# Kernel tuning notes

Measured on AMD Instinct MI355X. Metric: run time of the kernel, lower is better.

The kernel has to match this reference:

```python
import jax, jax.numpy as jnp
import numpy as np

MAX_THRESHOLD = 0.25  # init kwarg
B, S, D, E = 8, 4096, 512, 8


def setup_inputs() -> dict:
    key = jax.random.key(0)
    ks = jax.random.split(key, 5)
    scale = 1.0 / np.sqrt(D)
    return {
        "inputs": jax.random.normal(ks[0], (B, S, D), dtype=jnp.float32),
        "W_gate": jax.random.normal(ks[1], (D, E), dtype=jnp.float32) * scale,
        "b_gate": jnp.zeros((E,), dtype=jnp.float32),
        "W_thr": jax.random.normal(ks[2], (D, 1), dtype=jnp.float32) * scale,
        "b_thr": jnp.zeros((1,), dtype=jnp.float32),
        "W_exp": jax.random.normal(ks[3], (E, D, D), dtype=jnp.float32) * scale,
        "b_exp": jnp.zeros((E, D), dtype=jnp.float32),
    }


def reference(inputs, W_gate, b_gate, W_thr, b_thr, W_exp, b_exp):
    d = inputs.shape[-1]
    x = inputs.reshape(-1, d)  # [T, D]
    # gating
    gate_logits = jax.nn.softmax(x @ W_gate + b_gate, axis=-1)          # [T, E]
    thresholds = jax.nn.sigmoid(x @ W_thr + b_thr) * MAX_THRESHOLD      # [T, 1]
    adapted = gate_logits - thresholds                                  # [T, E]
    selected = (adapted >= 0).astype(x.dtype)                           # [T, E]
    weights = adapted * selected                                        # [T, E]
    wsum = jnp.sum(weights, axis=-1, keepdims=True)
    wsum = jnp.where(wsum == 0, jnp.ones_like(wsum), wsum)
    weights = weights / wsum
    # dense-equivalent of gather->expert->scatter (weights are 0 where unselected)
    ex_out = jnp.einsum('td,edf->etf', x, W_exp) + b_exp[:, None, :]    # [E, T, D]
    results = jnp.einsum('etf,te->tf', ex_out, weights)                 # [T, D]
    return results.reshape(inputs.shape[:-1] + (results.shape[-1],))
```

## Files before the change

kernel.cpp:

```cpp
#include <hip/hip_runtime.h>


#define T_TOKENS 32768
#define DDIM 512
#define KDIM 4096
#define SLOTB 16384
#define SLOTA 16384

typedef __attribute__((ext_vector_type(8))) short short8;
typedef __attribute__((ext_vector_type(4))) float floatx4;
typedef __bf16 bf16x2 __attribute__((ext_vector_type(2)));

__device__ __forceinline__ unsigned short f2bf(float f) {
    unsigned int u = __float_as_uint(f);
    u += 0x7FFFu + ((u >> 16) & 1u);
    return (unsigned short)(u >> 16);
}

__device__ __forceinline__ unsigned int pk2(float a, float b) {
#if __has_builtin(__builtin_amdgcn_cvt_pk_bf16_f32)
    bf16x2 v = __builtin_amdgcn_cvt_pk_bf16_f32(a, b);
    return __builtin_bit_cast(unsigned int, v);
#else
    return (unsigned int)f2bf(a) | ((unsigned int)f2bf(b) << 16);
#endif
}

__device__ __forceinline__ void async_copy16(const void* g, void* l) {
    __builtin_amdgcn_global_load_lds(
        (const __attribute__((address_space(1))) void*)g,
        (__attribute__((address_space(3))) void*)l, 16, 0, 0);
}

__device__ __forceinline__ unsigned int scale_pair(unsigned int u, float w) {
    float lo = __uint_as_float(u << 16) * w;
    float hi = __uint_as_float(u & 0xFFFF0000u) * w;
    return pk2(lo, hi);
}

__global__ __launch_bounds__(256) void gating_cvt_bt(
    const float* __restrict__ x, const float* __restrict__ Wg,
    const float* __restrict__ bg, const float* __restrict__ Wt,
    const float* __restrict__ bt, float* __restrict__ wbuf,
    unsigned short* __restrict__ Xbf,
    const float* __restrict__ Wexp, unsigned short* __restrict__ Bt)
{
    const int tid = threadIdx.x;

    if (blockIdx.x >= 512) {
        __shared__ float tile[64][65];
        const int bb = blockIdx.x - 512;
        const int k0 = (bb & 63) * 64;
        const int n0 = (bb >> 6) * 64;
        const int r = tid >> 4, cq = tid & 15;
#pragma unroll
        for (int p = 0; p < 4; ++p) {
            const int rr = p * 16 + r;
            const float4 v = *(const float4*)(Wexp + (size_t)(k0 + rr) * 512 + n0 + cq * 4);
            tile[rr][cq * 4 + 0] = v.x;
            tile[rr][cq * 4 + 1] = v.y;
            tile[rr][cq * 4 + 2] = v.z;
            tile[rr][cq * 4 + 3] = v.w;
        }
        __syncthreads();
        const int rn = tid >> 2;
        const int kq = tid & 3;
        alignas(16) unsigned short buf[16];
#pragma unroll
        for (int j = 0; j < 16; ++j) buf[j] = f2bf(tile[kq * 16 + j][rn]);
        unsigned short* dst = Bt + (size_t)(n0 + rn) * KDIM + k0 + kq * 16;
        *(uint4*)(dst) = *(const uint4*)(buf);
        *(uint4*)(dst + 8) = *(const uint4*)(buf + 8);
        return;
    }

    const int wv = tid >> 6;
    const int lane = tid & 63;

    float4 wg[16];
    {
        const float4* wgp = (const float4*)(Wg + lane * 64);
#pragma unroll
        for (int c = 0; c < 16; ++c) wg[c] = wgp[c];
    }
    const float4 wt0 = *(const float4*)(Wt + lane * 8);
    const float4 wt1 = *(const float4*)(Wt + lane * 8 + 4);
    const float bgv[8] = {bg[0], bg[1], bg[2], bg[3], bg[4], bg[5], bg[6], bg[7]};
    const float btv = bt[0];

    for (int it = 0; it < 16; ++it) {
        const int t = blockIdx.x * 64 + wv * 16 + it;
        const float* xp = x + (size_t)t * 512 + lane * 8;
        const float4 a0 = *(const float4*)(xp);
        const float4 a1 = *(const float4*)(xp + 4);

        uint2 pk0, pk1;
        pk0.x = pk2(a0.x, a0.y);
        pk0.y = pk2(a0.z, a0.w);
        pk1.x = pk2(a1.x, a1.y);
        pk1.y = pk2(a1.z, a1.w);
        uint2* xd = (uint2*)(Xbf + (size_t)t * 512 + lane * 8);
        xd[0] = pk0;
        xd[1] = pk1;

        const float xv[8] = {a0.x, a0.y, a0.z, a0.w, a1.x, a1.y, a1.z, a1.w};
        const float wtv[8] = {wt0.x, wt0.y, wt0.z, wt0.w, wt1.x, wt1.y, wt1.z, wt1.w};
        float g[9];
#pragma unroll
        for (int e = 0; e < 9; ++e) g[e] = 0.f;
#pragma unroll
        for (int j = 0; j < 8; ++j) {
            const float4 wlo = wg[j * 2];
            const float4 whi = wg[j * 2 + 1];
            g[0] = fmaf(xv[j], wlo.x, g[0]);
            g[1] = fmaf(xv[j], wlo.y, g[1]);
            g[2] = fmaf(xv[j], wlo.z, g[2]);
            g[3] = fmaf(xv[j], wlo.w, g[3]);
            g[4] = fmaf(xv[j], whi.x, g[4]);
            g[5] = fmaf(xv[j], whi.y, g[5]);
            g[6] = fmaf(xv[j], whi.z, g[6]);
            g[7] = fmaf(xv[j], whi.w, g[7]);
            g[8] = fmaf(xv[j], wtv[j], g[8]);
        }
#pragma unroll
        for (int e = 0; e < 9; ++e) {
            g[e] += __shfl_xor(g[e], 1);
            g[e] += __shfl_xor(g[e], 2);
            g[e] += __shfl_xor(g[e], 4);
            g[e] += __shfl_xor(g[e], 8);
            g[e] += __shfl_xor(g[e], 16);
            g[e] += __shfl_xor(g[e], 32);
        }
        if (lane == 0) {
#pragma unroll
            for (int e = 0; e < 8; ++e) g[e] += bgv[e];
            g[8] += btv;
            float m = g[0];
#pragma unroll
            for (int e = 1; e < 8; ++e) m = fmaxf(m, g[e]);
            float s = 0.f;
            float p[8];
#pragma unroll
            for (int e = 0; e < 8; ++e) { p[e] = __expf(g[e] - m); s += p[e]; }
            const float inv = 1.f / s;
            const float thr = 0.25f / (1.f + __expf(-g[8]));
            float w8[8];
            float ws = 0.f;
#pragma unroll
            for (int e = 0; e < 8; ++e) {
                float a = p[e] * inv - thr;
                w8[e] = a > 0.f ? a : 0.f;
                ws += w8[e];
            }
            if (ws == 0.f) ws = 1.f;
            const float invw = 1.f / ws;
            float4 o0, o1;
            o0.x = w8[0] * invw; o0.y = w8[1] * invw; o0.z = w8[2] * invw; o0.w = w8[3] * invw;
            o1.x = w8[4] * invw; o1.y = w8[5] * invw; o1.z = w8[6] * invw; o1.w = w8[7] * invw;
            float4* op = (float4*)(wbuf + (size_t)t * 8);
            op[0] = o0;
            op[1] = o1;
        }
    }
}

__global__ __launch_bounds__(512, 2) void moe_gemm(
    const unsigned short* __restrict__ Xbf, const float* __restrict__ wbuf,
    const float* __restrict__ bexp, const unsigned short* __restrict__ Bt,
    float* __restrict__ out)
{
    __shared__ alignas(16) unsigned short Bs[3 * SLOTB];
    __shared__ alignas(16) unsigned short As[SLOTA];
    __shared__ float sWbT[8 * 256];

    const int tid = threadIdx.x;
    const int wave = tid >> 6;
    const int lane = tid & 63;
    const int wm = wave >> 2;
    const int wn = wave & 3;
    const int lm = lane & 15;
    const int lq = lane >> 4;
    const int brow = lane >> 3;
    const int cg = (lane & 7) ^ brow;
    const int c8 = tid & 7;
    const int r0 = tid >> 3;
    const int swzA = ((c8 ^ (r0 & 7)) << 3);

    const int lin = blockIdx.x;
    const int g = lin & 7;
    const int j_ = lin >> 3;
    const int t0 = (g * 16 + (j_ >> 1)) * 256;
    const int n0 = (j_ & 1) * 256;

    {
        const int row = tid & 255, pr = tid >> 8;
        const float4 w4 = *(const float4*)(wbuf + (size_t)(t0 + row) * 8 + pr * 4);
        sWbT[(pr * 4 + 0) * 256 + row] = w4.x;
        sWbT[(pr * 4 + 1) * 256 + row] = w4.y;
        sWbT[(pr * 4 + 2) * 256 + row] = w4.z;
        sWbT[(pr * 4 + 3) * 256 + row] = w4.w;
    }

#define STAGE_B(s_, slot_, i0, i1)                                              \
    {                                                                           \
        const int k0_ = (s_) << 6;                                              \
        _Pragma("unroll")                                                       \
        for (int i = (i0); i < (i1); ++i)                                       \
            async_copy16(Bt + (size_t)(n0 + wave * 32 + i * 8 + brow) * KDIM + k0_ + cg * 8, \
                         Bs + (slot_) * SLOTB + (wave * 32 + i * 8) * 64);      \
    }
#define LOADA_ISSUE(s_)                                                         \
    {                                                                           \
        const int d0_ = ((s_) & 7) << 6;                                        \
        _Pragma("unroll")                                                       \
        for (int m = 0; m < 4; ++m)                                             \
            ar[m] = *(const uint4*)(Xbf + (size_t)(t0 + r0 + m * 64) * 512 + d0_ + c8 * 8); \
    }
#define ASCALE_WRITE(s_)                                                        \
    {                                                                           \
        const int e1 = (s_) >> 3;                                               \
        _Pragma("unroll")                                                       \
        for (int m = 0; m < 4; ++m) {                                           \
            const float w = sWbT[e1 * 256 + r0 + m * 64];                       \
            uint4 o;                                                            \
            o.x = scale_pair(ar[m].x, w);                                       \
            o.y = scale_pair(ar[m].y, w);                                       \
            o.z = scale_pair(ar[m].z, w);                                       \
            o.w = scale_pair(ar[m].w, w);                                       \
            *(uint4*)(As + (r0 + m * 64) * 64 + swzA) = o;                      \
        }                                                                       \
    }
#define READ_A(ih)                                                              \
    {                                                                           \
        _Pragma("unroll")                                                       \
        for (int ii = 0; ii < 4; ++ii)                                          \
            _Pragma("unroll")                                                   \
            for (int kk = 0; kk < 2; ++kk) {                                    \
                const int row = wm * 128 + ((ih) * 4 + ii) * 16 + lm;           \
                const int ch = kk * 4 + lq;                                     \
                af[ii][kk] = *(const short8*)(As + row * 64 + ((ch ^ (row & 7)) << 3)); \
            }                                                                   \
    }
#define READ_B(q_, dst)                                                         \
    {                                                                           \
        _Pragma("unroll")                                                       \
        for (int jj = 0; jj < 2; ++jj)                                          \
            _Pragma("unroll")                                                   \
            for (int kk = 0; kk < 2; ++kk) {                                    \
                const int row = wn * 64 + ((q_) * 2 + jj) * 16 + lm;            \
                const int ch = kk * 4 + lq;                                     \
                dst[jj][kk] = *(const short8*)(Bb + row * 64 + ((ch ^ (row & 7)) << 3)); \
            }                                                                   \
    }
#define MFMA_Q(ih, q_, bq)                                                      \
    {                                                                           \
        __builtin_amdgcn_s_setprio(1);                                          \
        _Pragma("unroll")                                                       \
        for (int ii = 0; ii < 4; ++ii)                                          \
            _Pragma("unroll")                                                   \
            for (int jj = 0; jj < 2; ++jj)                                      \
                _Pragma("unroll")                                               \
                for (int kk = 0; kk < 2; ++kk)                                  \
                    acc[(ih) * 4 + ii][(q_) * 2 + jj] =                         \
                        __builtin_amdgcn_mfma_f32_16x16x32_bf16(                \
                            af[ii][kk], bq[jj][kk], acc[(ih) * 4 + ii][(q_) * 2 + jj], 0, 0, 0); \
        __builtin_amdgcn_s_setprio(0);                                          \
    }

    floatx4 acc[8][4];
#pragma unroll
    for (int i = 0; i < 8; ++i)
#pragma unroll
        for (int j = 0; j < 4; ++j) acc[i][j] = (floatx4){0.f, 0.f, 0.f, 0.f};

    uint4 ar[4];

    LOADA_ISSUE(0);
    STAGE_B(0, 0, 0, 4);
    STAGE_B(1, 1, 0, 4);
    asm volatile("s_waitcnt vmcnt(8)" ::: "memory");
    ASCALE_WRITE(0);
    asm volatile("s_waitcnt vmcnt(4) lgkmcnt(0)" ::: "memory");
    __builtin_amdgcn_s_barrier();

    int sB = 0;
    for (int s = 0; s < 64; ++s) {
        const int sB1 = (sB == 2) ? 0 : sB + 1;
        const int sB2 = (sB == 0) ? 2 : sB - 1;
        const unsigned short* Bb = Bs + sB * SLOTB;
        short8 af[4][2], b0[2][2], b1[2][2];

        READ_A(0);
        READ_B(0, b0);
        if (s < 63) LOADA_ISSUE(s + 1);
        __builtin_amdgcn_s_barrier();
        MFMA_Q(0, 0, b0);
        __builtin_amdgcn_s_barrier();

        READ_B(1, b1);
        if (s < 62) STAGE_B(s + 2, sB2, 0, 2);
        __builtin_amdgcn_s_barrier();
        MFMA_Q(0, 1, b1);
        __builtin_amdgcn_s_barrier();

        READ_A(1);
        if (s < 62) STAGE_B(s + 2, sB2, 2, 4);
        __builtin_amdgcn_s_barrier();
        MFMA_Q(1, 1, b1);
        __builtin_amdgcn_s_barrier();

        if (s < 62) {
            asm volatile("s_waitcnt vmcnt(4)" ::: "memory");
        } else if (s == 62) {
            asm volatile("s_waitcnt vmcnt(0)" ::: "memory");
        }
        if (s < 63) ASCALE_WRITE(s + 1);
        READ_B(0, b0);
        __builtin_amdgcn_s_barrier();
        MFMA_Q(1, 0, b0);
        asm volatile("s_waitcnt lgkmcnt(0)" ::: "memory");
        __builtin_amdgcn_s_barrier();

        sB = sB1;
    }

    float bc[4][8];
#pragma unroll
    for (int j = 0; j < 4; ++j) {
        const int col = n0 + wn * 64 + j * 16 + lm;
#pragma unroll
        for (int e = 0; e < 8; ++e) bc[j][e] = bexp[e * 512 + col];
    }
#pragma unroll
    for (int i = 0; i < 8; ++i)
#pragma unroll
        for (int r = 0; r < 4; ++r) {
            const int rowl = wm * 128 + i * 16 + lq * 4 + r;
            const float4 w0 = *(const float4*)(wbuf + (size_t)(t0 + rowl) * 8);
            const float4 w1 = *(const float4*)(wbuf + (size_t)(t0 + rowl) * 8 + 4);
            float* op = out + (size_t)(t0 + rowl) * 512 + n0 + wn * 64 + lm;
#pragma unroll
            for (int j = 0; j < 4; ++j) {
                float bias = w0.x * bc[j][0];
                bias = fmaf(w0.y, bc[j][1], bias);
                bias = fmaf(w0.z, bc[j][2], bias);
                bias = fmaf(w0.w, bc[j][3], bias);
                bias = fmaf(w1.x, bc[j][4], bias);
                bias = fmaf(w1.y, bc[j][5], bias);
                bias = fmaf(w1.z, bc[j][6], bias);
                bias = fmaf(w1.w, bc[j][7], bias);
                op[j * 16] = acc[i][j][r] + bias;
            }
        }
#undef STAGE_B
#undef LOADA_ISSUE
#undef ASCALE_WRITE
#undef READ_A
#undef READ_B
#undef MFMA_Q
}

extern "C" void kernel_launch(void* const* d_in, const int* in_sizes, int n_in,
                              void* d_out, int out_size, void* d_ws, size_t ws_size,
                              hipStream_t stream) {
    const float* x   = (const float*)d_in[0];
    const float* Wg  = (const float*)d_in[1];
    const float* bg  = (const float*)d_in[2];
    const float* Wt  = (const float*)d_in[3];
    const float* bt  = (const float*)d_in[4];
    const float* Wex = (const float*)d_in[5];
    const float* bex = (const float*)d_in[6];
    float* out = (float*)d_out;

    unsigned short* Xbf = (unsigned short*)d_ws;
    unsigned short* Bt  = (unsigned short*)((char*)d_ws + (size_t)T_TOKENS * DDIM * 2);
    float* wbuf = (float*)((char*)d_ws + (size_t)T_TOKENS * DDIM * 2
                                       + (size_t)DDIM * KDIM * 2);

    gating_cvt_bt<<<1024, 256, 0, stream>>>(x, Wg, bg, Wt, bt, wbuf, Xbf, Wex, Bt);
    moe_gemm<<<256, 512, 0, stream>>>(Xbf, wbuf, bex, Bt, out);
}
```

Measured before the change: 282.7 us.

## Halve GEMM K-step to 32 with double-buffered A and smaller LDS slots

Restructures the MoE GEMM main loop from 64 steps of K=64 into 128 steps of K=32. The B tile keeps three slots and the scaled A tile now has two slots, each half the previous size, with a new 4-chunk XOR swizzle. LDS use drops from about 136 KB to about 88 KB, and each step runs two MFMA halves with fewer barriers per step. This cuts shared memory pressure, which may allow two blocks per CU, at the cost of twice as many loop iterations and synchronisation points.

Result: slower. 310.2 us (+9.7%).

```diff
diff --git a/kernel.cpp b/kernel.cpp
--- a/kernel.cpp
+++ b/kernel.cpp
@@ -4,8 +4,7 @@
 #define T_TOKENS 32768
 #define DDIM 512
 #define KDIM 4096
-#define SLOTB 16384
-#define SLOTA 16384
+#define SLOT32 8192
 
 typedef __attribute__((ext_vector_type(8))) short short8;
 typedef __attribute__((ext_vector_type(4))) float floatx4;
@@ -169,8 +168,8 @@
     const float* __restrict__ bexp, const unsigned short* __restrict__ Bt,
     float* __restrict__ out)
 {
-    __shared__ alignas(16) unsigned short Bs[3 * SLOTB];
-    __shared__ alignas(16) unsigned short As[SLOTA];
+    __shared__ alignas(16) unsigned short Bs[3 * SLOT32];
+    __shared__ alignas(16) unsigned short Asl[2 * SLOT32];
     __shared__ float sWbT[8 * 256];
 
     const int tid = threadIdx.x;
@@ -180,11 +179,10 @@
     const int wn = wave & 3;
     const int lm = lane & 15;
     const int lq = lane >> 4;
-    const int brow = lane >> 3;
-    const int cg = (lane & 7) ^ brow;
-    const int c8 = tid & 7;
-    const int r0 = tid >> 3;
-    const int swzA = ((c8 ^ (r0 & 7)) << 3);
+    const int srow = wave * 16 + (lane >> 2);
+    const int pc = lane & 3;
+    const int cgk = pc ^ ((lane >> 3) & 3);
+    const int prd = lq ^ ((lm >> 1) & 3);
 
     const int lin = blockIdx.x;
     const int g = lin & 7;
@@ -201,69 +199,59 @@
         sWbT[(pr * 4 + 3) * 256 + row] = w4.w;
     }
 
-#define STAGE_B(s_, slot_, i0, i1)                                              \
-    {                                                                           \
-        const int k0_ = (s_) << 6;                                              \
-        _Pragma("unroll")                                                       \
-        for (int i = (i0); i < (i1); ++i)                                       \
-            async_copy16(Bt + (size_t)(n0 + wave * 32 + i * 8 + brow) * KDIM + k0_ + cg * 8, \
-                         Bs + (slot_) * SLOTB + (wave * 32 + i * 8) * 64);      \
-    }
-#define LOADA_ISSUE(s_)                                                         \
-    {                                                                           \
-        const int d0_ = ((s_) & 7) << 6;                                        \
-        _Pragma("unroll")                                                       \
-        for (int m = 0; m < 4; ++m)                                             \
-            ar[m] = *(const uint4*)(Xbf + (size_t)(t0 + r0 + m * 64) * 512 + d0_ + c8 * 8); \
-    }
-#define ASCALE_WRITE(s_)                                                        \
-    {                                                                           \
-        const int e1 = (s_) >> 3;                                               \
-        _Pragma("unroll")                                                       \
-        for (int m = 0; m < 4; ++m) {                                           \
-            const float w = sWbT[e1 * 256 + r0 + m * 64];                       \
+#define STAGE_B(s_, slot_)                                                      \
+    {                                                                           \
+        _Pragma("unroll")                                                       \
+        for (int i = 0; i < 2; ++i)                                             \
+            async_copy16(Bt + (size_t)(n0 + i * 128 + srow) * KDIM + (s_) * 32 + cgk * 8, \
+                         Bs + (slot_) * SLOT32 + (i * 128 + wave * 16) * 32);   \
+    }
+#define LOADA(s_)                                                               \
+    {                                                                           \
+        const int d0_ = ((s_) & 15) << 5;                                       \
+        _Pragma("unroll")                                                       \
+        for (int i = 0; i < 2; ++i)                                             \
+            ar[i] = *(const uint4*)(Xbf + (size_t)(t0 + i * 128 + srow) * 512 + d0_ + pc * 8); \
+    }
+#define AWRITE(s_)                                                              \
+    {                                                                           \
+        const int e1 = (s_) >> 4;                                               \
+        _Pragma("unroll")                                                       \
+        for (int i = 0; i < 2; ++i) {                                           \
+            const float w = sWbT[e1 * 256 + i * 128 + srow];                    \
             uint4 o;                                                            \
-            o.x = scale_pair(ar[m].x, w);                                       \
-            o.y = scale_pair(ar[m].y, w);                                       \
-            o.z = scale_pair(ar[m].z, w);                                       \
-            o.w = scale_pair(ar[m].w, w);                                       \
-            *(uint4*)(As + (r0 + m * 64) * 64 + swzA) = o;                      \
+            o.x = scale_pair(ar[i].x, w);                                       \
+            o.y = scale_pair(ar[i].y, w);                                       \
+            o.z = scale_pair(ar[i].z, w);                                       \
+            o.w = scale_pair(ar[i].w, w);                                       \
+            *(uint4*)(Asl + ((s_) & 1) * SLOT32 + (i * 128 + srow) * 32 + cgk * 8) = o; \
         }                                                                       \
     }
-#define READ_A(ih)                                                              \
-    {                                                                           \
+#define READ_AF(ih)                                                             \
+    {                                                                           \
+        _Pragma("unroll")                                                       \
+        for (int ii = 0; ii < 4; ++ii) {                                        \
+            const int row = wm * 128 + ((ih) * 4 + ii) * 16 + lm;               \
+            af[ii] = *(const short8*)(Ab + row * 32 + prd * 8);                 \
+        }                                                                       \
+    }
+#define READ_B()                                                                \
+    {                                                                           \
+        _Pragma("unroll")                                                       \
+        for (int j = 0; j < 4; ++j) {                                           \
+            const int row = wn * 64 + j * 16 + lm;                              \
+            b[j] = *(const short8*)(Bb + row * 32 + prd * 8);                   \
+        }                                                                       \
+    }
+#define MFMA_H(ih)                                                              \
+    {                                                                           \
+        __builtin_amdgcn_s_setprio(1);                                          \
         _Pragma("unroll")                                                       \
         for (int ii = 0; ii < 4; ++ii)                                          \
             _Pragma("unroll")                                                   \
-            for (int kk = 0; kk < 2; ++kk) {                                    \
-                const int row = wm * 128 + ((ih) * 4 + ii) * 16 + lm;           \
-                const int ch = kk * 4 + lq;                                     \
-                af[ii][kk] = *(const short8*)(As + row * 64 + ((ch ^ (row & 7)) << 3)); \
-            }                                                                   \
-    }
-#define READ_B(q_, dst)                                                         \
-    {                                                                           \
-        _Pragma("unroll")                                                       \
-        for (int jj = 0; jj < 2; ++jj)                                          \
-            _Pragma("unroll")                                                   \
-            for (int kk = 0; kk < 2; ++kk) {                                    \
-                const int row = wn * 64 + ((q_) * 2 + jj) * 16 + lm;            \
-                const int ch = kk * 4 + lq;                                     \
-                dst[jj][kk] = *(const short8*)(Bb + row * 64 + ((ch ^ (row & 7)) << 3)); \
-            }                                                                   \
-    }
-#define MFMA_Q(ih, q_, bq)                                                      \
-    {                                                                           \
-        __builtin_amdgcn_s_setprio(1);                                          \
-        _Pragma("unroll")                                                       \
-        for (int ii = 0; ii < 4; ++ii)                                          \
-            _Pragma("unroll")                                                   \
-            for (int jj = 0; jj < 2; ++jj)                                      \
-                _Pragma("unroll")                                               \
-                for (int kk = 0; kk < 2; ++kk)                                  \
-                    acc[(ih) * 4 + ii][(q_) * 2 + jj] =                         \
-                        __builtin_amdgcn_mfma_f32_16x16x32_bf16(                \
-                            af[ii][kk], bq[jj][kk], acc[(ih) * 4 + ii][(q_) * 2 + jj], 0, 0, 0); \
+            for (int j = 0; j < 4; ++j)                                         \
+                acc[(ih) * 4 + ii][j] = __builtin_amdgcn_mfma_f32_16x16x32_bf16( \
+                    af[ii], b[j], acc[(ih) * 4 + ii][j], 0, 0, 0);              \
         __builtin_amdgcn_s_setprio(0);                                          \
     }
 
@@ -273,55 +261,44 @@
 #pragma unroll
         for (int j = 0; j < 4; ++j) acc[i][j] = (floatx4){0.f, 0.f, 0.f, 0.f};
 
-    uint4 ar[4];
-
-    LOADA_ISSUE(0);
-    STAGE_B(0, 0, 0, 4);
-    STAGE_B(1, 1, 0, 4);
-    asm volatile("s_waitcnt vmcnt(8)" ::: "memory");
-    ASCALE_WRITE(0);
-    asm volatile("s_waitcnt vmcnt(4) lgkmcnt(0)" ::: "memory");
+    uint4 ar[2];
+
+    LOADA(0);
+    STAGE_B(0, 0);
+    STAGE_B(1, 1);
+    __syncthreads();
+    AWRITE(0);
+    asm volatile("s_waitcnt lgkmcnt(0)" ::: "memory");
     __builtin_amdgcn_s_barrier();
 
-    int sB = 0;
-    for (int s = 0; s < 64; ++s) {
-        const int sB1 = (sB == 2) ? 0 : sB + 1;
-        const int sB2 = (sB == 0) ? 2 : sB - 1;
-        const unsigned short* Bb = Bs + sB * SLOTB;
-        short8 af[4][2], b0[2][2], b1[2][2];
-
-        READ_A(0);
-        READ_B(0, b0);
-        if (s < 63) LOADA_ISSUE(s + 1);
+    int sl = 0;
+    for (int s = 0; s < 128; ++s) {
+        const unsigned short* Ab = Asl + (s & 1) * SLOT32;
+        const unsigned short* Bb = Bs + sl * SLOT32;
+        const int sl2 = (sl == 0) ? 2 : sl - 1;
+        short8 af[4], b[4];
+
+        READ_AF(0);
+        READ_B();
+        if (s < 127) LOADA(s + 1);
+        if (s < 126) STAGE_B(s + 2, sl2);
         __builtin_amdgcn_s_barrier();
-        MFMA_Q(0, 0, b0);
+        MFMA_H(0);
         __builtin_amdgcn_s_barrier();
 
-        READ_B(1, b1);
-        if (s < 62) STAGE_B(s + 2, sB2, 0, 2);
+        READ_AF(1);
+        if (s < 126) {
+            asm volatile("s_waitcnt vmcnt(2)" ::: "memory");
+        } else if (s == 126) {
+            asm volatile("s_waitcnt vmcnt(0)" ::: "memory");
+        }
+        if (s < 127) AWRITE(s + 1);
         __builtin_amdgcn_s_barrier();
-        MFMA_Q(0, 1, b1);
+        MFMA_H(1);
+        if (s < 127) asm volatile("s_waitcnt lgkmcnt(0)" ::: "memory");
         __builtin_amdgcn_s_barrier();
 
-        READ_A(1);
-        if (s < 62) STAGE_B(s + 2, sB2, 2, 4);
-        __builtin_amdgcn_s_barrier();
-        MFMA_Q(1, 1, b1);
-        __builtin_amdgcn_s_barrier();
-
-        if (s < 62) {
-            asm volatile("s_waitcnt vmcnt(4)" ::: "memory");
-        } else if (s == 62) {
-            asm volatile("s_waitcnt vmcnt(0)" ::: "memory");
-        }
-        if (s < 63) ASCALE_WRITE(s + 1);
-        READ_B(0, b0);
-        __builtin_amdgcn_s_barrier();
-        MFMA_Q(1, 0, b0);
-        asm volatile("s_waitcnt lgkmcnt(0)" ::: "memory");
-        __builtin_amdgcn_s_barrier();
-
-        sB = sB1;
+        sl = (sl == 2) ? 0 : sl + 1;
     }
 
     float bc[4][8];
@@ -353,11 +330,11 @@
             }
         }
 #undef STAGE_B
-#undef LOADA_ISSUE
-#undef ASCALE_WRITE
-#undef READ_A
+#undef LOADA
+#undef AWRITE
+#undef READ_AF
 #undef READ_B
-#undef MFMA_Q
+#undef MFMA_H
 }
 
 extern "C" void kernel_launch(void* const* d_in, const int* in_sizes, int n_in,
```
